# Optimization experiments

Hardware: AMD Instinct MI355X
Metric: run time of the kernel (lower is better)

The kernel has to match this reference:

```python
import jax, jax.numpy as jnp
import jax.scipy.linalg as jsl
import numpy as np

B, T, C = 2, 4096, 1024
HK = HV = 8           # linear_num_key_heads == linear_num_value_heads
DK = DV = 128         # linear_key_head_dim / linear_value_head_dim
CHUNK = 64
CONV_K = 4
KEY_DIM = HK * DK
VAL_DIM = HV * DV
CONV_DIM = 2 * KEY_DIM + VAL_DIM
EPS = 1e-6


def setup_inputs() -> dict:
    key = jax.random.key(0)
    ks = jax.random.split(key, 8)
    s = 0.02
    x = jax.random.normal(ks[0], (B, T, C), jnp.float32)
    W_qkvz = jax.random.normal(ks[1], (C, 2 * KEY_DIM + 2 * VAL_DIM), jnp.float32) * s
    W_ba = jax.random.normal(ks[2], (C, 2 * HV), jnp.float32) * s
    conv_w = jax.random.normal(ks[3], (CONV_DIM, 1, CONV_K), jnp.float32) * 0.3  # depthwise (O,1,K)
    dt_bias = jnp.ones((HV,), jnp.float32)
    A_log = jnp.log(jax.random.uniform(ks[4], (HV,), jnp.float32, 0.5, 8.0))
    norm_weight = jnp.ones((DV,), jnp.float32)
    W_out = jax.random.normal(ks[5], (VAL_DIM, C), jnp.float32) * s
    return {"x": x, "W_qkvz": W_qkvz, "W_ba": W_ba, "conv_w": conv_w,
            "dt_bias": dt_bias, "A_log": A_log, "norm_weight": norm_weight, "W_out": W_out}


def _l2norm(x, eps=EPS):
    return x * jax.lax.rsqrt(jnp.sum(x * x, -1, keepdims=True) + eps)


def _chunk_gated_delta_rule(q, k, v, g, beta, chunk=CHUNK):
    # q,k: (B,T,H,DK); v: (B,T,H,DV); g,beta: (B,T,H)
    q = _l2norm(q)
    k = _l2norm(k)
    tr = lambda x: jnp.swapaxes(x, 1, 2).astype(jnp.float32)  # -> (B,H,T,...)
    q, k, v, g, beta = tr(q), tr(k), tr(v), tr(g), tr(beta)
    b, h, t, dk = k.shape
    dv = v.shape[-1]
    n = t // chunk  # T divisible by chunk (pad_size == 0)
    q = q * (dk ** -0.5)
    v_beta = v * beta[..., None]
    k_beta = k * beta[..., None]
    rs = lambda x: x.reshape(b, h, n, chunk, x.shape[-1])
    q, k, v_beta, k_beta = rs(q), rs(k), rs(v_beta), rs(k_beta)
    g = jnp.cumsum(g.reshape(b, h, n, chunk), axis=-1)
    # decay_mask[..., i, j] = exp(g_i - g_j) for j <= i, else 0
    decay = jnp.tril(jnp.exp(jnp.tril(g[..., :, None] - g[..., None, :])))
    # forward substitution == unit-lower-triangular solve: (I + tri)^{-1}
    tri = jnp.tril(jnp.einsum('bhnck,bhndk->bhncd', k_beta, k) * decay, -1)
    eye = jnp.eye(chunk, dtype=jnp.float32)
    Tm = jsl.solve_triangular(eye + tri, jnp.broadcast_to(eye, tri.shape), lower=True)
    v_new = Tm @ v_beta                                   # (B,H,N,C,DV)
    k_cum = Tm @ (k_beta * jnp.exp(g)[..., None])         # (B,H,N,C,DK)
    keep_low = jnp.tril(jnp.ones((chunk, chunk), bool))

    def step(S, inp):
        q_i, k_i, v_i, kc_i, g_i, dm_i = inp              # (B,H,C,*)
        attn = jnp.where(keep_low, (q_i @ jnp.swapaxes(k_i, -1, -2)) * dm_i, 0.0)
        v_n = v_i - kc_i @ S
        out = (q_i * jnp.exp(g_i)[..., None]) @ S + attn @ v_n
        g_last = g_i[..., -1]
        S = S * jnp.exp(g_last)[..., None, None] + jnp.einsum(
            'bhck,bhcv->bhkv', k_i * jnp.exp(g_last[..., None] - g_i)[..., None], v_n)
        return S, out

    mv = lambda x: jnp.moveaxis(x, 2, 0)                  # chunk axis to front
    S0 = jnp.zeros((b, h, dk, dv), jnp.float32)
    S, outs = jax.lax.scan(step, S0, (mv(q), mv(k), mv(v_new), mv(k_cum), mv(g), mv(decay)))
    out = jnp.moveaxis(outs, 0, 2).reshape(b, h, t, dv)
    return jnp.swapaxes(out, 1, 2), S                     # (B,T,H,DV), (B,H,DK,DV)


def reference(x, W_qkvz, W_ba, conv_w, dt_bias, A_log, norm_weight, W_out):
    Bx, Tx, Cx = x.shape
    ratio = HV // HK
    qkvz = (x @ W_qkvz).reshape(Bx, Tx, HK, 2 * DK + 2 * ratio * DV)
    q, k, v, z = jnp.split(qkvz, [DK, 2 * DK, 2 * DK + ratio * DV], axis=3)
    v = v.reshape(Bx, Tx, HV, DV)
    z = z.reshape(Bx, Tx, HV, DV)
    ba = (x @ W_ba).reshape(Bx, Tx, HK, 2 * ratio)
    b_, a_ = jnp.split(ba, [ratio], axis=3)
    b_ = b_.reshape(Bx, Tx, HV)
    a_ = a_.reshape(Bx, Tx, HV)
    mixed = jnp.concatenate([q.reshape(Bx, Tx, -1), k.reshape(Bx, Tx, -1),
                             v.reshape(Bx, Tx, -1)], axis=-1)
    # causal depthwise conv1d (left pad K-1, take first T)
    xc = jnp.swapaxes(mixed, 1, 2)                        # (B, CONV_DIM, T)
    conv = jax.lax.conv_general_dilated(xc, conv_w, (1,), [(CONV_K - 1, 0)],
                                        dimension_numbers=('NCH', 'OIH', 'NCH'),
                                        feature_group_count=CONV_DIM)
    conv = jnp.swapaxes(jax.nn.silu(conv), 1, 2)          # (B,T,CONV_DIM)
    qc, kc, vc = jnp.split(conv, [KEY_DIM, 2 * KEY_DIM], axis=-1)
    qc = qc.reshape(Bx, Tx, HK, DK)
    kc = kc.reshape(Bx, Tx, HK, DK)
    vc = vc.reshape(Bx, Tx, HV, DV)
    if ratio > 1:
        qc = jnp.repeat(qc, ratio, axis=2)
        kc = jnp.repeat(kc, ratio, axis=2)
    beta = jax.nn.sigmoid(b_)
    g = -jnp.exp(A_log) * jax.nn.softplus(a_ + dt_bias)
    core, _ = _chunk_gated_delta_rule(qc, kc, vc, g, beta)
    # GatedRMSNorm over head_v_dim, gated by silu(z)
    h = core.astype(jnp.float32)
    var = jnp.mean(h * h, -1, keepdims=True)
    h = norm_weight * (h * jax.lax.rsqrt(var + EPS))
    h = h * jax.nn.silu(z.astype(jnp.float32))
    return h.reshape(Bx, Tx, VAL_DIM) @ W_out
```

## Files before the change

kernel.cpp:

```cpp
#include <hip/hip_runtime.h>
#include <cstddef>

#define Bx 2
#define Tn 4096
#define Hh 8

typedef unsigned short u16;
typedef unsigned int u32;
typedef __attribute__((ext_vector_type(8))) short short8;
typedef __attribute__((ext_vector_type(4))) float f32x4;

__device__ __forceinline__ float bf2f(u16 u) {
  u32 x = ((u32)u) << 16;
  return __uint_as_float(x);
}
__device__ __forceinline__ u16 f2bf(float f) {
  u32 x = __float_as_uint(f);
  u32 lsb = (x >> 16) & 1;
  x += 0x7fffu + lsb;
  return (u16)(x >> 16);
}
__device__ __forceinline__ u32 pack2(float a, float b) {
  return (u32)f2bf(a) | ((u32)f2bf(b) << 16);
}
__device__ __forceinline__ short8 cvt8(float4 f0, float4 f1) {
  uint4 p;
  p.x = pack2(f0.x, f0.y);
  p.y = pack2(f0.z, f0.w);
  p.z = pack2(f1.x, f1.y);
  p.w = pack2(f1.z, f1.w);
  return *(short8*)&p;
}
__device__ __forceinline__ void async16(u16* lds, const u16* g) {
  __builtin_amdgcn_global_load_lds((const __attribute__((address_space(1))) void*)g,
                                   (__attribute__((address_space(3))) void*)lds, 16, 0, 0);
}

__global__ __launch_bounds__(256) void conv_bf16(const float* __restrict__ X,
                                                 u16* __restrict__ Xb) {
  int i = (blockIdx.x * 256 + threadIdx.x) * 8;
  float4 v0 = *(const float4*)&X[i];
  float4 v1 = *(const float4*)&X[i + 4];
  uint4 pv;
  pv.x = pack2(v0.x, v0.y);
  pv.y = pack2(v0.z, v0.w);
  pv.z = pack2(v1.x, v1.y);
  pv.w = pack2(v1.z, v1.w);
  *(uint4*)&Xb[i] = pv;
}

__global__ __launch_bounds__(256) void transpose_bf16(const float* __restrict__ W,
                                                      u16* __restrict__ WT,
                                                      int K, int N) {
  __shared__ float tile[64][68];
  int nb = blockIdx.x, kb = blockIdx.y;
  int tid = threadIdx.x;
  int r = tid >> 4, c4 = (tid & 15) * 4;
#pragma unroll
  for (int p = 0; p < 4; p++) {
    int k = kb * 64 + p * 16 + r;
    float4 v = *(const float4*)&W[(size_t)k * N + nb * 64 + c4];
    tile[p * 16 + r][c4] = v.x;
    tile[p * 16 + r][c4 + 1] = v.y;
    tile[p * 16 + r][c4 + 2] = v.z;
    tile[p * 16 + r][c4 + 3] = v.w;
  }
  __syncthreads();
  int rn = tid >> 2, ck = (tid & 3) * 16;
#pragma unroll
  for (int s = 0; s < 2; s++) {
    int k0 = ck + s * 8;
    uint4 pv;
    pv.x = pack2(tile[k0 + 0][rn], tile[k0 + 1][rn]);
    pv.y = pack2(tile[k0 + 2][rn], tile[k0 + 3][rn]);
    pv.z = pack2(tile[k0 + 4][rn], tile[k0 + 5][rn]);
    pv.w = pack2(tile[k0 + 6][rn], tile[k0 + 7][rn]);
    *(uint4*)&WT[(size_t)(nb * 64 + rn) * K + kb * 64 + k0] = pv;
  }
}

template<int EPI>
__global__ __launch_bounds__(256) void gemm_mfma(const u16* __restrict__ A,
                                                 const u16* __restrict__ Bt,
                                                 u16* __restrict__ O1,
                                                 u16* __restrict__ O2,
                                                 float* __restrict__ O3,
                                                 int Nfull) {
  const int K = 1024;
  __shared__ u16 As[128 * 32];
  __shared__ u16 Bs[128 * 32];
  int bn = blockIdx.x, bm = blockIdx.y;
  int tid = threadIdx.x;
  int wave = tid >> 6, lane = tid & 63;
  int wr = wave >> 1, wc = wave & 1;

  f32x4 acc[4][4];
#pragma unroll
  for (int i = 0; i < 4; i++)
#pragma unroll
    for (int j = 0; j < 4; j++) acc[i][j] = (f32x4){0.f, 0.f, 0.f, 0.f};

  const u16* Ab = A + (size_t)(bm * 128 + wave * 32 + (lane >> 2)) * K + (lane & 3) * 8;
  const u16* Bb = Bt + (size_t)(bn * 128 + wave * 32 + (lane >> 2)) * K + (lane & 3) * 8;
  u16* AsW = &As[(wave * 32) * 32];
  u16* BsW = &Bs[(wave * 32) * 32];

  int m_lane = lane & 15, k_lane = (lane >> 4) * 8;
  const u16* arow0 = &As[(wr * 64 + m_lane) * 32 + k_lane];
  const u16* brow0 = &Bs[(wc * 64 + m_lane) * 32 + k_lane];

  for (int kk = 0; kk < K; kk += 32) {
    __syncthreads();
    async16(AsW, Ab + kk);
    async16(AsW + 16 * 32, Ab + 16 * K + kk);
    async16(BsW, Bb + kk);
    async16(BsW + 16 * 32, Bb + 16 * K + kk);
    __syncthreads();
    short8 a[4], b[4];
#pragma unroll
    for (int t = 0; t < 4; t++) a[t] = *(const short8*)(arow0 + t * 16 * 32);
#pragma unroll
    for (int t = 0; t < 4; t++) b[t] = *(const short8*)(brow0 + t * 16 * 32);
#pragma unroll
    for (int i = 0; i < 4; i++)
#pragma unroll
      for (int j = 0; j < 4; j++)
        acc[i][j] = __builtin_amdgcn_mfma_f32_16x16x32_bf16(a[i], b[j], acc[i][j], 0, 0, 0);
  }

  int n0 = bn * 128;
  int cbase = wc * 64 + (lane & 15);
  int rbase = bm * 128 + wr * 64 + ((lane >> 4) * 4);
  if (EPI == 1) {
    int h = n0 >> 9, sub = (n0 >> 7) & 3;
    u16* dst;
    size_t stride;
    if (sub < 3) { dst = O1 + (size_t)(sub * 1024 + h * 128); stride = 3072; }
    else         { dst = O2 + (size_t)(h * 128);              stride = 1024; }
#pragma unroll
    for (int i = 0; i < 4; i++)
#pragma unroll
      for (int j = 0; j < 4; j++)
#pragma unroll
        for (int r = 0; r < 4; r++)
          dst[(size_t)(rbase + i * 16 + r) * stride + cbase + j * 16] = f2bf(acc[i][j][r]);
  } else {
#pragma unroll
    for (int i = 0; i < 4; i++)
#pragma unroll
      for (int j = 0; j < 4; j++)
#pragma unroll
        for (int r = 0; r < 4; r++)
          O3[(size_t)(rbase + i * 16 + r) * Nfull + n0 + cbase + j * 16] = acc[i][j][r];
  }
}

__global__ __launch_bounds__(128) void ba_kernel(const float* __restrict__ x,
                                                 const float* __restrict__ Wba,
                                                 const float* __restrict__ dtb,
                                                 const float* __restrict__ Alog,
                                                 float* __restrict__ betab,
                                                 float* __restrict__ gb) {
  __shared__ float xs[1024];
  __shared__ float part[8][16];
  int row = blockIdx.x, tid = threadIdx.x;
#pragma unroll
  for (int r = 0; r < 2; r++) {
    int f4 = r * 128 + tid;
    *(float4*)&xs[f4 * 4] = *(const float4*)&x[(size_t)row * 1024 + f4 * 4];
  }
  __syncthreads();
  int col = tid & 15, seg = tid >> 4;
  float a = 0.f;
  for (int k = seg * 128; k < seg * 128 + 128; k++) a += xs[k] * Wba[k * 16 + col];
  part[seg][col] = a;
  __syncthreads();
  if (tid < 8) {
    float bval = 0.f, aval = 0.f;
#pragma unroll
    for (int q = 0; q < 8; q++) { bval += part[q][tid * 2]; aval += part[q][tid * 2 + 1]; }
    betab[(size_t)row * 8 + tid] = 1.f / (1.f + expf(-bval));
    float spin = aval + dtb[tid];
    float sp = (spin > 20.f) ? spin : log1pf(expf(spin));
    gb[(size_t)row * 8 + tid] = -expf(Alog[tid]) * sp;
  }
}

__global__ __launch_bounds__(256) void convnorm(const u16* __restrict__ mixed,
                                                const float* __restrict__ cw,
                                                const float* __restrict__ gbuf,
                                                u16* __restrict__ qn,
                                                u16* __restrict__ kn,
                                                u16* __restrict__ kdT) {
  __shared__ __align__(16) u16 sRaw[67 * 128];
  __shared__ __align__(16) u16 sO[64 * 136];
  __shared__ float red_s[256];
  __shared__ float inv_s[64];
  __shared__ float eglc_s[64];
  int n = blockIdx.x, bh = blockIdx.y, type = blockIdx.z;
  int b = bh >> 3, h = bh & 7;
  int t0 = n * 64, tid = threadIdx.x;
  int srow = tid >> 4, scol8 = (tid & 15) * 8;
  int base = type * 1024;

#pragma unroll
  for (int pass = 0; pass < 5; pass++) {
    int r = pass * 16 + srow;
    if (r < 67) {
      int t = t0 - 3 + r;
      uint4 v = make_uint4(0u, 0u, 0u, 0u);
      if (t >= 0) v = *(const uint4*)&mixed[(size_t)(b * Tn + t) * 3072 + base + h * 128 + scol8];
      *(uint4*)&sRaw[r * 128 + scol8] = v;
    }
  }
  if (type == 1 && tid < 64) {
    float gv = gbuf[(size_t)(b * Tn + t0 + tid) * 8 + h];
#pragma unroll
    for (int off = 1; off < 64; off <<= 1) {
      float o = __shfl_up(gv, off, 64);
      if (tid >= off) gv += o;
    }
    float gl = __shfl(gv, 63, 64);
    eglc_s[tid] = expf(gl - gv);
  }
  __syncthreads();

#pragma unroll
  for (int it = 0; it < 32; it++) {
    int idx = it * 256 + tid;
    int i = idx >> 7, d = idx & 127;
    int colw = (base + h * 128 + d) * 4;
    float a = 0.f;
#pragma unroll
    for (int tap = 0; tap < 4; tap++)
      a += bf2f(sRaw[(i + tap) * 128 + d]) * cw[colw + tap];
    a = a / (1.f + expf(-a));
    sO[i * 136 + d] = f2bf(a);
  }
  __syncthreads();
  {
    int i = tid >> 2, p = tid & 3;
    float ss = 0.f;
#pragma unroll
    for (int d = p * 32; d < p * 32 + 32; d += 2) {
      u32 w2 = *(const u32*)&sO[i * 136 + d];
      float a = bf2f(w2 & 0xffff), b2 = bf2f(w2 >> 16);
      ss += a * a + b2 * b2;
    }
    red_s[tid] = ss;
  }
  __syncthreads();
  if (tid < 64) {
    float inv = rsqrtf(red_s[tid * 4] + red_s[tid * 4 + 1] + red_s[tid * 4 + 2] + red_s[tid * 4 + 3] + 1e-6f);
    inv_s[tid] = (type == 0) ? inv * 0.08838834764831845f : inv;
  }
  __syncthreads();
  u16* dstRow = (type == 0 ? qn : kn) + (size_t)(bh * Tn + t0) * 128;
#pragma unroll
  for (int it = 0; it < 16; it++) {
    int idx = it * 256 + tid;
    int i = idx >> 6, d2 = (idx & 63) * 2;
    u32 w2 = *(const u32*)&sO[i * 136 + d2];
    float inv = inv_s[i];
    float q0 = bf2f(w2 & 0xffff) * inv, q1 = bf2f(w2 >> 16) * inv;
    u32 pk = pack2(q0, q1);
    if (type == 1) *(u32*)&sO[i * 136 + d2] = pk;
    *(u32*)&dstRow[(size_t)i * 128 + d2] = pk;
  }
  if (type == 1) {
    __syncthreads();
    const size_t tbase = (size_t)(bh * 64 + n) * 8192;
#pragma unroll
    for (int it = 0; it < 32; it++) {
      int idx = it * 256 + tid;
      int d = idx >> 6, i = idx & 63;
      kdT[tbase + d * 64 + i] = f2bf(bf2f(sO[i * 136 + d]) * eglc_s[i]);
    }
  }
}

__global__ __launch_bounds__(256) void prep(const u16* __restrict__ mixed,
                                            const float* __restrict__ cw,
                                            const float* __restrict__ gbuf,
                                            const float* __restrict__ betabuf,
                                            u16* qbuf,
                                            u16* kbuf,
                                            u16* __restrict__ vnT,
                                            u16* __restrict__ attn,
                                            float* __restrict__ egl) {
  __shared__ __align__(16) u16 sKn[64 * 136];
  __shared__ __align__(16) u16 sQn[64 * 136];
  __shared__ __align__(16) u16 sRawV[67 * 128];
  __shared__ float gc_s[64], egc_s[64], bet_s[64];
  float* triL = (float*)sQn;

  int n = blockIdx.x, bh = blockIdx.y;
  int b = bh >> 3, h = bh & 7;
  int t0 = n * 64;
  int tid = threadIdx.x;
  const int rowg0 = b * Tn + t0;
  const int rowh0 = bh * Tn + t0;
  const size_t tbase = (size_t)(bh * 64 + n) * 8192;

  int wv = tid >> 6, lane = tid & 63;
  int m16 = lane & 15, q8 = (lane >> 4) * 8, qr = (lane >> 4) * 4;
  int srow = tid >> 4, scol8 = (tid & 15) * 8;

#pragma unroll
  for (int it = 0; it < 4; it++) {
    int idx = it * 256 + tid;
    int i = idx >> 4, c8 = (idx & 15) * 8;
    *(uint4*)&sQn[i * 136 + c8] = *(const uint4*)&qbuf[(size_t)(rowh0 + i) * 128 + c8];
    *(uint4*)&sKn[i * 136 + c8] = *(const uint4*)&kbuf[(size_t)(rowh0 + i) * 128 + c8];
  }
#pragma unroll
  for (int pass = 0; pass < 5; pass++) {
    int r = pass * 16 + srow;
    if (r < 67) {
      int t = t0 - 3 + r;
      uint4 v = make_uint4(0u, 0u, 0u, 0u);
      if (t >= 0) v = *(const uint4*)&mixed[(size_t)(b * Tn + t) * 3072 + 2048 + h * 128 + scol8];
      *(uint4*)&sRawV[r * 128 + scol8] = v;
    }
  }
  if (tid < 64) {
    float gv = gbuf[(size_t)(rowg0 + tid) * 8 + h];
    float bv = betabuf[(size_t)(rowg0 + tid) * 8 + h];
#pragma unroll
    for (int off = 1; off < 64; off <<= 1) {
      float o = __shfl_up(gv, off, 64);
      if (tid >= off) gv += o;
    }
    float gl = __shfl(gv, 63, 64);
    gc_s[tid] = gv;
    egc_s[tid] = expf(gv);
    bet_s[tid] = bv;
    if (tid == 63) egl[bh * 64 + n] = expf(gl);
  }
  __syncthreads();

#pragma unroll
  for (int it = 0; it < 16; it++) {
    int idx = it * 256 + tid;
    int i = idx >> 6, d2 = (idx & 63) * 2;
    u32 w2 = *(const u32*)&sQn[i * 136 + d2];
    float e = egc_s[i];
    *(u32*)&qbuf[(size_t)(rowh0 + i) * 128 + d2] =
        pack2(bf2f(w2 & 0xffff) * e, bf2f(w2 >> 16) * e);
  }
  {
    short8 qa[4];
#pragma unroll
    for (int kt = 0; kt < 4; kt++)
      qa[kt] = *(const short8*)&sQn[(wv * 16 + m16) * 136 + kt * 32 + q8];
    u16* atp = attn + (size_t)(bh * 64 + n) * 4096;
#pragma unroll
    for (int jt = 0; jt < 4; jt++) {
      int j = jt * 16 + m16;
      if (jt <= wv) {
        f32x4 o = (f32x4){0.f, 0.f, 0.f, 0.f};
#pragma unroll
        for (int kt = 0; kt < 4; kt++) {
          short8 kb = *(const short8*)&sKn[(jt * 16 + m16) * 136 + kt * 32 + q8];
          o = __builtin_amdgcn_mfma_f32_16x16x32_bf16(qa[kt], kb, o, 0, 0, 0);
        }
#pragma unroll
        for (int r = 0; r < 4; r++) {
          int i = wv * 16 + qr + r;
          float val = (j <= i) ? o[r] * expf(gc_s[i] - gc_s[j]) : 0.f;
          atp[i * 64 + j] = f2bf(val);
        }
      } else {
#pragma unroll
        for (int r = 0; r < 4; r++) atp[(wv * 16 + qr + r) * 64 + j] = 0;
      }
    }
  }
  __syncthreads();
  {
    short8 ka[4];
#pragma unroll
    for (int kt = 0; kt < 4; kt++)
      ka[kt] = *(const short8*)&sKn[(wv * 16 + m16) * 136 + kt * 32 + q8];
#pragma unroll
    for (int jt = 0; jt < 4; jt++) {
      int j = jt * 16 + m16;
      if (jt <= wv) {
        f32x4 o = (f32x4){0.f, 0.f, 0.f, 0.f};
#pragma unroll
        for (int kt = 0; kt < 4; kt++) {
          short8 kb = *(const short8*)&sKn[(jt * 16 + m16) * 136 + kt * 32 + q8];
          o = __builtin_amdgcn_mfma_f32_16x16x32_bf16(ka[kt], kb, o, 0, 0, 0);
        }
#pragma unroll
        for (int r = 0; r < 4; r++) {
          int i = wv * 16 + qr + r;
          triL[i * 64 + j] = (j < i) ? bet_s[i] * expf(gc_s[i] - gc_s[j]) * o[r] : 0.f;
        }
      } else if (jt == wv + 1) {
#pragma unroll
        for (int r = 0; r < 4; r++) triL[(wv * 16 + qr + r) * 64 + j] = 0.f;
      }
    }
  }
  __syncthreads();

  {
    int mat = tid >> 7, c = tid & 127;
    float x[64];
    if (mat == 0) {
#pragma unroll
      for (int i = 0; i < 64; i++)
        x[i] = bf2f(sKn[i * 136 + c]) * bet_s[i] * egc_s[i];
    } else {
      float cwv[4];
      int colw = (2048 + h * 128 + c) * 4;
#pragma unroll
      for (int tap = 0; tap < 4; tap++) cwv[tap] = cw[colw + tap];
#pragma unroll
      for (int i = 0; i < 64; i++) {
        float a = 0.f;
#pragma unroll
        for (int tap = 0; tap < 4; tap++)
          a += bf2f(sRawV[(i + tap) * 128 + c]) * cwv[tap];
        a = a / (1.f + expf(-a));
        x[i] = a * bet_s[i];
      }
    }
#pragma unroll
    for (int i = 1; i < 64; i++) {
      float s0 = 0.f, s1 = 0.f, s2 = 0.f, s3 = 0.f;
#pragma unroll
      for (int l4 = 0; l4 < (i + 3) / 4; l4++) {
        float4 t4 = *(float4*)&triL[i * 64 + l4 * 4];
        s0 += t4.x * x[l4 * 4 + 0];
        s1 += t4.y * x[l4 * 4 + 1];
        s2 += t4.z * x[l4 * 4 + 2];
        s3 += t4.w * x[l4 * 4 + 3];
      }
      x[i] = x[i] - ((s0 + s1) + (s2 + s3));
    }
    if (mat == 0) {
#pragma unroll
      for (int i = 0; i < 64; i++) kbuf[(size_t)(rowh0 + i) * 128 + c] = f2bf(-x[i]);
    } else {
#pragma unroll
      for (int i = 0; i < 64; i += 2)
        *(u32*)&vnT[tbase + c * 64 + i] = pack2(x[i], x[i + 1]);
    }
  }
}

__device__ __forceinline__ void stage_half(int w, u16* ldsb,
                                           const u16* __restrict__ qgc,
                                           const u16* __restrict__ kcc,
                                           const u16* __restrict__ ktc,
                                           const u16* __restrict__ atc,
                                           const u16* __restrict__ vtc,
                                           int lane) {
  int l8 = lane * 8;
  if (w == 0) {
#pragma unroll
    for (int i = 0; i < 16; i++) {
      int p = i * 512 + l8;
      async16(ldsb + i * 512, qgc + (p ^ ((((p >> 7) & 15)) << 3)));
    }
#pragma unroll
    for (int i = 0; i < 8; i++) {
      int p = i * 512 + l8;
      async16(ldsb + 24576 + i * 512, atc + (p ^ ((((p >> 6) & 7)) << 3)));
    }
#pragma unroll
    for (int i = 0; i < 2; i++) {
      int p = i * 512 + l8;
      async16(ldsb + 28672 + i * 512, vtc + (p ^ ((((p >> 6) & 7)) << 3)));
    }
  } else {
#pragma unroll
    for (int i = 0; i < 16; i++) {
      int p = i * 512 + l8;
      async16(ldsb + 8192 + i * 512, kcc + (p ^ ((((p >> 7) & 15)) << 3)));
    }
#pragma unroll
    for (int i = 0; i < 16; i++) {
      int p = i * 512 + l8;
      async16(ldsb + 16384 + i * 512, ktc + (p ^ ((((p >> 6) & 7)) << 3)));
    }
  }
}

__global__ __launch_bounds__(128, 1) void scan_mfma(const u16* __restrict__ qg,
                                                    const u16* __restrict__ kdT,
                                                    const u16* __restrict__ vnT,
                                                    const u16* __restrict__ kcum,
                                                    const u16* __restrict__ attn,
                                                    const float* __restrict__ egl,
                                                    float* __restrict__ core) {
  extern __shared__ __align__(16) u16 dyn[];
  __shared__ float ST[16 * 132];
  __shared__ float VN[16 * 68];
  int blk = blockIdx.x;
  int bh = blk & 15, tile = blk >> 4;
  int dv0 = tile * 16;
  int b = bh >> 3, h = bh & 7;
  int tid = threadIdx.x;
  int w = tid >> 6, lane = tid & 63;
  int q = lane >> 4, col = lane & 15;
  int c7 = col & 7;
  int tw0 = w * 4;

  for (int r = tid; r < 16 * 132; r += 128) ST[r] = 0.f;
  float egAll = egl[bh * 64 + lane];

  const u16* qg_base = qg + (size_t)bh * Tn * 128;
  const u16* kc_base = kcum + (size_t)bh * Tn * 128;
  const u16* kt_base = kdT + (size_t)bh * 64 * 8192;
  const u16* at_base = attn + (size_t)bh * 64 * 4096;
  const u16* vt_base = vnT + (size_t)bh * 64 * 8192 + dv0 * 64;

  stage_half(w, dyn, qg_base, kc_base, kt_base, at_base, vt_base, lane);
  asm volatile("s_waitcnt vmcnt(0)" ::: "memory");
  __syncthreads();

  for (int n = 0; n < 64; n++) {
    u16* buf = dyn + (n & 1) * 29696;

    short8 kcf[8], qgf[8], ktf[8], atf[4];
    uint2 vtf[2];
#pragma unroll
    for (int m = 0; m < 2; m++) {
      int mt = w * 2 + m;
#pragma unroll
      for (int kt = 0; kt < 4; kt++) {
        kcf[m * 4 + kt] = *(const short8*)&buf[8192 + (mt * 16 + col) * 128 +
                                               (((kt * 4 + q) ^ col) << 3)];
        qgf[m * 4 + kt] = *(const short8*)&buf[(mt * 16 + col) * 128 +
                                               (((kt * 4 + q) ^ col) << 3)];
      }
#pragma unroll
      for (int kt2 = 0; kt2 < 2; kt2++)
        atf[m * 2 + kt2] = *(const short8*)&buf[24576 + (mt * 16 + col) * 64 +
                                                (((kt2 * 4 + q) ^ c7) << 3)];
      vtf[m] = *(const uint2*)&buf[28672 + col * 64 +
                                   (((mt * 2 + (q >> 1)) ^ c7) << 3) + (q & 1) * 4];
    }
#pragma unroll
    for (int t = 0; t < 4; t++)
#pragma unroll
      for (int kt2 = 0; kt2 < 2; kt2++)
        ktf[t * 2 + kt2] = *(const short8*)&buf[16384 + ((tw0 + t) * 16 + col) * 64 +
                                                (((kt2 * 4 + q) ^ c7) << 3)];
    short8 sb[4];
#pragma unroll
    for (int kt = 0; kt < 4; kt++) {
      float4 f0 = *(float4*)&ST[col * 132 + kt * 32 + q * 8];
      float4 f1 = *(float4*)&ST[col * 132 + kt * 32 + q * 8 + 4];
      sb[kt] = cvt8(f0, f1);
    }
    float4 stu[4];
#pragma unroll
    for (int t = 0; t < 4; t++) stu[t] = *(float4*)&ST[col * 132 + (tw0 + t) * 16 + q * 4];

    if (n < 63) {
      stage_half(w, dyn + ((n + 1) & 1) * 29696,
                 qg_base + (size_t)(n + 1) * 8192,
                 kc_base + (size_t)(n + 1) * 8192,
                 kt_base + (size_t)(n + 1) * 8192,
                 at_base + (size_t)(n + 1) * 4096,
                 vt_base + (size_t)(n + 1) * 8192, lane);
    }
    float eg = __shfl(egAll, n, 64);

#pragma unroll
    for (int m = 0; m < 2; m++) {
      f32x4 a0;
      a0[0] = bf2f(vtf[m].x & 0xffff); a0[1] = bf2f(vtf[m].x >> 16);
      a0[2] = bf2f(vtf[m].y & 0xffff); a0[3] = bf2f(vtf[m].y >> 16);
#pragma unroll
      for (int kt = 0; kt < 4; kt++)
        a0 = __builtin_amdgcn_mfma_f32_16x16x32_bf16(kcf[m * 4 + kt], sb[kt], a0, 0, 0, 0);
      *(f32x4*)&VN[col * 68 + (w * 2 + m) * 16 + q * 4] = a0;
    }
    asm volatile("s_waitcnt lgkmcnt(0)" ::: "memory");
    __builtin_amdgcn_s_barrier();
    __builtin_amdgcn_sched_barrier(0);

    short8 vb[2];
#pragma unroll
    for (int kt2 = 0; kt2 < 2; kt2++) {
      float4 f0 = *(float4*)&VN[col * 68 + kt2 * 32 + q * 8];
      float4 f1 = *(float4*)&VN[col * 68 + kt2 * 32 + q * 8 + 4];
      vb[kt2] = cvt8(f0, f1);
    }

#pragma unroll
    for (int t = 0; t < 4; t++) {
      f32x4 s0;
      s0[0] = stu[t].x * eg; s0[1] = stu[t].y * eg;
      s0[2] = stu[t].z * eg; s0[3] = stu[t].w * eg;
#pragma unroll
      for (int kt2 = 0; kt2 < 2; kt2++)
        s0 = __builtin_amdgcn_mfma_f32_16x16x32_bf16(ktf[t * 2 + kt2], vb[kt2], s0, 0, 0, 0);
      *(f32x4*)&ST[col * 132 + (tw0 + t) * 16 + q * 4] = s0;
    }

#pragma unroll
    for (int m = 0; m < 2; m++) {
      f32x4 o = (f32x4){0.f, 0.f, 0.f, 0.f};
#pragma unroll
      for (int kt = 0; kt < 4; kt++)
        o = __builtin_amdgcn_mfma_f32_16x16x32_bf16(qgf[m * 4 + kt], sb[kt], o, 0, 0, 0);
#pragma unroll
      for (int kt2 = 0; kt2 < 2; kt2++)
        o = __builtin_amdgcn_mfma_f32_16x16x32_bf16(atf[m * 2 + kt2], vb[kt2], o, 0, 0, 0);
      size_t rowb = (size_t)(b * Tn) + n * 64 + (w * 2 + m) * 16 + q * 4;
#pragma unroll
      for (int r2 = 0; r2 < 4; r2++)
        core[(rowb + r2) * 1024 + h * 128 + dv0 + col] = o[r2];
    }

    asm volatile("s_waitcnt vmcnt(8) lgkmcnt(0)" ::: "memory");
    __builtin_amdgcn_s_barrier();
    __builtin_amdgcn_sched_barrier(0);
  }
}

__global__ __launch_bounds__(256) void gnorm(const float* __restrict__ core,
                                             const u16* __restrict__ z,
                                             const float* __restrict__ nw,
                                             u16* __restrict__ coreb) {
  __shared__ float red[256];
  __shared__ float rstd[8];
  int row = blockIdx.x, tid = threadIdx.x;
  float4 c4 = *(const float4*)&core[(size_t)row * 1024 + tid * 4];
  uint2 zl = *(const uint2*)&z[(size_t)row * 1024 + tid * 4];
  float4 z4;
  z4.x = bf2f(zl.x & 0xffff); z4.y = bf2f(zl.x >> 16);
  z4.z = bf2f(zl.y & 0xffff); z4.w = bf2f(zl.y >> 16);
  red[tid] = c4.x * c4.x + c4.y * c4.y + c4.z * c4.z + c4.w * c4.w;
  __syncthreads();
  if (tid < 8) {
    float s = 0.f;
    for (int t2 = tid * 32; t2 < tid * 32 + 32; t2++) s += red[t2];
    rstd[tid] = rsqrtf(s * (1.f / 128.f) + 1e-6f);
  }
  __syncthreads();
  float rs = rstd[tid >> 5];
  int d0 = (tid * 4) & 127;
  float4 w4 = *(const float4*)&nw[d0];
  float4 o;
  o.x = c4.x * rs * w4.x * (z4.x / (1.f + expf(-z4.x)));
  o.y = c4.y * rs * w4.y * (z4.y / (1.f + expf(-z4.y)));
  o.z = c4.z * rs * w4.z * (z4.z / (1.f + expf(-z4.z)));
  o.w = c4.w * rs * w4.w * (z4.w / (1.f + expf(-z4.w)));
  uint2 pv;
  pv.x = pack2(o.x, o.y);
  pv.y = pack2(o.z, o.w);
  *(uint2*)&coreb[(size_t)row * 1024 + tid * 4] = pv;
}

extern "C" void kernel_launch(void* const* d_in, const int* in_sizes, int n_in,
                              void* d_out, int out_size, void* d_ws, size_t ws_size,
                              hipStream_t stream) {
  const float* x     = (const float*)d_in[0];
  const float* Wqkvz = (const float*)d_in[1];
  const float* Wba   = (const float*)d_in[2];
  const float* convw = (const float*)d_in[3];
  const float* dtb   = (const float*)d_in[4];
  const float* Alog  = (const float*)d_in[5];
  const float* nw    = (const float*)d_in[6];
  const float* Wout  = (const float*)d_in[7];
  float* out = (float*)d_out;

  char* w = (char*)d_ws;
  u16*   mixed = (u16*)w;
  float* core  = (float*)w;
  u16*   coreb = (u16*)(w + 33554432);
  u16*   zb    = (u16*)(w + 50331648);
  float* betab = (float*)(w + 67108864);
  float* gb    = (float*)(w + 67371008);
  u16*   qgB   = (u16*)(w + 67633152);
  u16*   xb    = (u16*)(w + 67633152);
  u16*   kdTB  = (u16*)(w + 84410368);
  u16*   WqT   = (u16*)(w + 84410368);
  u16*   vnTB  = (u16*)(w + 101187584);
  u16*   kcB   = (u16*)(w + 117964800);
  u16*   WoT   = (u16*)(w + 117964800);
  u16*   atB   = (u16*)(w + 134742016);
  float* eglB  = (float*)(w + 143130624);

  static bool attr_set = false;
  if (!attr_set) {
    hipFuncSetAttribute(reinterpret_cast<const void*>(scan_mfma),
                        hipFuncAttributeMaxDynamicSharedMemorySize, 118784);
    attr_set = true;
  }

  conv_bf16<<<dim3(4096), 256, 0, stream>>>(x, xb);
  transpose_bf16<<<dim3(64, 16), 256, 0, stream>>>(Wqkvz, WqT, 1024, 4096);
  gemm_mfma<1><<<dim3(32, 64), 256, 0, stream>>>(xb, WqT, mixed, zb, nullptr, 4096);
  ba_kernel<<<dim3(8192), 128, 0, stream>>>(x, Wba, dtb, Alog, betab, gb);
  convnorm<<<dim3(64, 16, 2), 256, 0, stream>>>(mixed, convw, gb, qgB, kcB, kdTB);
  prep<<<dim3(64, 16), 256, 0, stream>>>(mixed, convw, gb, betab, qgB, kcB, vnTB, atB, eglB);
  scan_mfma<<<dim3(128), 128, 118784, stream>>>(qgB, kdTB, vnTB, kcB, atB, eglB, core);
  transpose_bf16<<<dim3(16, 16), 256, 0, stream>>>(Wout, WoT, 1024, 1024);
  gnorm<<<dim3(8192), 256, 0, stream>>>(core, zb, nw, coreb);
  gemm_mfma<0><<<dim3(8, 64), 256, 0, stream>>>(coreb, WoT, nullptr, nullptr, out, 1024);
}
```

Measured before the change: 446.3 us.

## Split scan work across four waves and keep state in registers with bf16 LDS

The sequential chunk-scan kernel now runs 4 waves per block instead of 2, so each wave owns one 16-row tile and half as many state tiles, and staging of the next chunk is split four ways. The fp32 recurrent state is kept in registers across iterations, and only a bf16, swizzled copy goes to LDS for the other waves to read. This removes the per-iteration fp32 LDS reads and conversions and shortens each wave's serial dependency chain. The cost is more barrier participants and extra bf16 packing work.

```diff
diff --git a/kernel.cpp b/kernel.cpp
--- a/kernel.cpp
+++ b/kernel.cpp
@@ -451,20 +451,33 @@
   }
 }
 
-__device__ __forceinline__ void stage_half(int w, u16* ldsb,
-                                           const u16* __restrict__ qgc,
-                                           const u16* __restrict__ kcc,
-                                           const u16* __restrict__ ktc,
-                                           const u16* __restrict__ atc,
-                                           const u16* __restrict__ vtc,
-                                           int lane) {
+__device__ __forceinline__ void stage_quarter(int w, u16* ldsb,
+                                              const u16* __restrict__ qgc,
+                                              const u16* __restrict__ kcc,
+                                              const u16* __restrict__ ktc,
+                                              const u16* __restrict__ atc,
+                                              const u16* __restrict__ vtc,
+                                              int lane) {
   int l8 = lane * 8;
   if (w == 0) {
+#pragma unroll
+    for (int i = 0; i < 16; i++) {
+      int p = i * 512 + l8;
+      async16(ldsb + 8192 + i * 512, kcc + (p ^ ((((p >> 7) & 15)) << 3)));
+    }
+  } else if (w == 1) {
+#pragma unroll
+    for (int i = 0; i < 16; i++) {
+      int p = i * 512 + l8;
+      async16(ldsb + 16384 + i * 512, ktc + (p ^ ((((p >> 6) & 7)) << 3)));
+    }
+  } else if (w == 2) {
 #pragma unroll
     for (int i = 0; i < 16; i++) {
       int p = i * 512 + l8;
       async16(ldsb + i * 512, qgc + (p ^ ((((p >> 7) & 15)) << 3)));
     }
+  } else {
 #pragma unroll
     for (int i = 0; i < 8; i++) {
       int p = i * 512 + l8;
@@ -475,21 +488,10 @@
       int p = i * 512 + l8;
       async16(ldsb + 28672 + i * 512, vtc + (p ^ ((((p >> 6) & 7)) << 3)));
     }
-  } else {
-#pragma unroll
-    for (int i = 0; i < 16; i++) {
-      int p = i * 512 + l8;
-      async16(ldsb + 8192 + i * 512, kcc + (p ^ ((((p >> 7) & 15)) << 3)));
-    }
-#pragma unroll
-    for (int i = 0; i < 16; i++) {
-      int p = i * 512 + l8;
-      async16(ldsb + 16384 + i * 512, ktc + (p ^ ((((p >> 6) & 7)) << 3)));
-    }
-  }
-}
-
-__global__ __launch_bounds__(128, 1) void scan_mfma(const u16* __restrict__ qg,
+  }
+}
+
+__global__ __launch_bounds__(256, 1) void scan_mfma(const u16* __restrict__ qg,
                                                     const u16* __restrict__ kdT,
                                                     const u16* __restrict__ vnT,
                                                     const u16* __restrict__ kcum,
@@ -497,8 +499,8 @@
                                                     const float* __restrict__ egl,
                                                     float* __restrict__ core) {
   extern __shared__ __align__(16) u16 dyn[];
-  __shared__ float ST[16 * 132];
-  __shared__ float VN[16 * 68];
+  __shared__ __align__(16) u16 STb[16 * 128];
+  __shared__ __align__(16) u16 VNb[16 * 64];
   int blk = blockIdx.x;
   int bh = blk & 15, tile = blk >> 4;
   int dv0 = tile * 16;
@@ -507,10 +509,13 @@
   int w = tid >> 6, lane = tid & 63;
   int q = lane >> 4, col = lane & 15;
   int c7 = col & 7;
-  int tw0 = w * 4;
-
-  for (int r = tid; r < 16 * 132; r += 128) ST[r] = 0.f;
+  int qh = q >> 1, ql = q & 1;
+
+  for (int r = tid; r < 16 * 128 / 2; r += 256) ((u32*)STb)[r] = 0u;
   float egAll = egl[bh * 64 + lane];
+
+  f32x4 st0 = (f32x4){0.f, 0.f, 0.f, 0.f};
+  f32x4 st1 = (f32x4){0.f, 0.f, 0.f, 0.f};
 
   const u16* qg_base = qg + (size_t)bh * Tn * 128;
   const u16* kc_base = kcum + (size_t)bh * Tn * 128;
@@ -518,68 +523,52 @@
   const u16* at_base = attn + (size_t)bh * 64 * 4096;
   const u16* vt_base = vnT + (size_t)bh * 64 * 8192 + dv0 * 64;
 
-  stage_half(w, dyn, qg_base, kc_base, kt_base, at_base, vt_base, lane);
+  stage_quarter(w, dyn, qg_base, kc_base, kt_base, at_base, vt_base, lane);
   asm volatile("s_waitcnt vmcnt(0)" ::: "memory");
   __syncthreads();
 
   for (int n = 0; n < 64; n++) {
     u16* buf = dyn + (n & 1) * 29696;
 
-    short8 kcf[8], qgf[8], ktf[8], atf[4];
-    uint2 vtf[2];
-#pragma unroll
-    for (int m = 0; m < 2; m++) {
-      int mt = w * 2 + m;
-#pragma unroll
-      for (int kt = 0; kt < 4; kt++) {
-        kcf[m * 4 + kt] = *(const short8*)&buf[8192 + (mt * 16 + col) * 128 +
-                                               (((kt * 4 + q) ^ col) << 3)];
-        qgf[m * 4 + kt] = *(const short8*)&buf[(mt * 16 + col) * 128 +
-                                               (((kt * 4 + q) ^ col) << 3)];
-      }
-#pragma unroll
-      for (int kt2 = 0; kt2 < 2; kt2++)
-        atf[m * 2 + kt2] = *(const short8*)&buf[24576 + (mt * 16 + col) * 64 +
+    short8 kcf[4], qgf[4], ktf[4], atf[2], sb[4];
+    uint2 vtf;
+#pragma unroll
+    for (int kt = 0; kt < 4; kt++) {
+      kcf[kt] = *(const short8*)&buf[8192 + (w * 16 + col) * 128 + (((kt * 4 + q) ^ col) << 3)];
+      qgf[kt] = *(const short8*)&buf[(w * 16 + col) * 128 + (((kt * 4 + q) ^ col) << 3)];
+      sb[kt] = *(const short8*)&STb[col * 128 + (((kt * 4 + q) ^ col) << 3)];
+    }
+#pragma unroll
+    for (int kt2 = 0; kt2 < 2; kt2++) {
+      atf[kt2] = *(const short8*)&buf[24576 + (w * 16 + col) * 64 + (((kt2 * 4 + q) ^ c7) << 3)];
+#pragma unroll
+      for (int t = 0; t < 2; t++)
+        ktf[t * 2 + kt2] = *(const short8*)&buf[16384 + ((w * 2 + t) * 16 + col) * 64 +
                                                 (((kt2 * 4 + q) ^ c7) << 3)];
-      vtf[m] = *(const uint2*)&buf[28672 + col * 64 +
-                                   (((mt * 2 + (q >> 1)) ^ c7) << 3) + (q & 1) * 4];
-    }
-#pragma unroll
-    for (int t = 0; t < 4; t++)
-#pragma unroll
-      for (int kt2 = 0; kt2 < 2; kt2++)
-        ktf[t * 2 + kt2] = *(const short8*)&buf[16384 + ((tw0 + t) * 16 + col) * 64 +
-                                                (((kt2 * 4 + q) ^ c7) << 3)];
-    short8 sb[4];
-#pragma unroll
-    for (int kt = 0; kt < 4; kt++) {
-      float4 f0 = *(float4*)&ST[col * 132 + kt * 32 + q * 8];
-      float4 f1 = *(float4*)&ST[col * 132 + kt * 32 + q * 8 + 4];
-      sb[kt] = cvt8(f0, f1);
-    }
-    float4 stu[4];
-#pragma unroll
-    for (int t = 0; t < 4; t++) stu[t] = *(float4*)&ST[col * 132 + (tw0 + t) * 16 + q * 4];
+    }
+    vtf = *(const uint2*)&buf[28672 + col * 64 + (((w * 2 + qh) ^ c7) << 3) + ql * 4];
 
     if (n < 63) {
-      stage_half(w, dyn + ((n + 1) & 1) * 29696,
-                 qg_base + (size_t)(n + 1) * 8192,
-                 kc_base + (size_t)(n + 1) * 8192,
-                 kt_base + (size_t)(n + 1) * 8192,
-                 at_base + (size_t)(n + 1) * 4096,
-                 vt_base + (size_t)(n + 1) * 8192, lane);
+      stage_quarter(w, dyn + ((n + 1) & 1) * 29696,
+                    qg_base + (size_t)(n + 1) * 8192,
+                    kc_base + (size_t)(n + 1) * 8192,
+                    kt_base + (size_t)(n + 1) * 8192,
+                    at_base + (size_t)(n + 1) * 4096,
+                    vt_base + (size_t)(n + 1) * 8192, lane);
     }
     float eg = __shfl(egAll, n, 64);
 
-#pragma unroll
-    for (int m = 0; m < 2; m++) {
+    {
       f32x4 a0;
-      a0[0] = bf2f(vtf[m].x & 0xffff); a0[1] = bf2f(vtf[m].x >> 16);
-      a0[2] = bf2f(vtf[m].y & 0xffff); a0[3] = bf2f(vtf[m].y >> 16);
+      a0[0] = bf2f(vtf.x & 0xffff); a0[1] = bf2f(vtf.x >> 16);
+      a0[2] = bf2f(vtf.y & 0xffff); a0[3] = bf2f(vtf.y >> 16);
 #pragma unroll
       for (int kt = 0; kt < 4; kt++)
-        a0 = __builtin_amdgcn_mfma_f32_16x16x32_bf16(kcf[m * 4 + kt], sb[kt], a0, 0, 0, 0);
-      *(f32x4*)&VN[col * 68 + (w * 2 + m) * 16 + q * 4] = a0;
+        a0 = __builtin_amdgcn_mfma_f32_16x16x32_bf16(kcf[kt], sb[kt], a0, 0, 0, 0);
+      uint2 pk;
+      pk.x = pack2(a0[0], a0[1]);
+      pk.y = pack2(a0[2], a0[3]);
+      *(uint2*)&VNb[col * 64 + (((w * 2 + qh) ^ c7) << 3) + ql * 4] = pk;
     }
     asm volatile("s_waitcnt lgkmcnt(0)" ::: "memory");
     __builtin_amdgcn_s_barrier();
@@ -587,39 +576,47 @@
 
     short8 vb[2];
 #pragma unroll
-    for (int kt2 = 0; kt2 < 2; kt2++) {
-      float4 f0 = *(float4*)&VN[col * 68 + kt2 * 32 + q * 8];
-      float4 f1 = *(float4*)&VN[col * 68 + kt2 * 32 + q * 8 + 4];
-      vb[kt2] = cvt8(f0, f1);
-    }
-
-#pragma unroll
-    for (int t = 0; t < 4; t++) {
+    for (int kt2 = 0; kt2 < 2; kt2++)
+      vb[kt2] = *(const short8*)&VNb[col * 64 + (((kt2 * 4 + q) ^ c7) << 3)];
+
+    {
       f32x4 s0;
-      s0[0] = stu[t].x * eg; s0[1] = stu[t].y * eg;
-      s0[2] = stu[t].z * eg; s0[3] = stu[t].w * eg;
+      s0[0] = st0[0] * eg; s0[1] = st0[1] * eg; s0[2] = st0[2] * eg; s0[3] = st0[3] * eg;
+      s0 = __builtin_amdgcn_mfma_f32_16x16x32_bf16(ktf[0], vb[0], s0, 0, 0, 0);
+      s0 = __builtin_amdgcn_mfma_f32_16x16x32_bf16(ktf[1], vb[1], s0, 0, 0, 0);
+      st0 = s0;
+      uint2 pk;
+      pk.x = pack2(s0[0], s0[1]);
+      pk.y = pack2(s0[2], s0[3]);
+      *(uint2*)&STb[col * 128 + ((((w * 2 + 0) * 2 + qh) ^ col) << 3) + ql * 4] = pk;
+    }
+    {
+      f32x4 s1;
+      s1[0] = st1[0] * eg; s1[1] = st1[1] * eg; s1[2] = st1[2] * eg; s1[3] = st1[3] * eg;
+      s1 = __builtin_amdgcn_mfma_f32_16x16x32_bf16(ktf[2], vb[0], s1, 0, 0, 0);
+      s1 = __builtin_amdgcn_mfma_f32_16x16x32_bf16(ktf[3], vb[1], s1, 0, 0, 0);
+      st1 = s1;
+      uint2 pk;
+      pk.x = pack2(s1[0], s1[1]);
+      pk.y = pack2(s1[2], s1[3]);
+      *(uint2*)&STb[col * 128 + ((((w * 2 + 1) * 2 + qh) ^ col) << 3) + ql * 4] = pk;
+    }
+
+    {
+      f32x4 o = (f32x4){0.f, 0.f, 0.f, 0.f};
+#pragma unroll
+      for (int kt = 0; kt < 4; kt++)
+        o = __builtin_amdgcn_mfma_f32_16x16x32_bf16(qgf[kt], sb[kt], o, 0, 0, 0);
 #pragma unroll
       for (int kt2 = 0; kt2 < 2; kt2++)
-        s0 = __builtin_amdgcn_mfma_f32_16x16x32_bf16(ktf[t * 2 + kt2], vb[kt2], s0, 0, 0, 0);
-      *(f32x4*)&ST[col * 132 + (tw0 + t) * 16 + q * 4] = s0;
-    }
-
-#pragma unroll
-    for (int m = 0; m < 2; m++) {
-      f32x4 o = (f32x4){0.f, 0.f, 0.f, 0.f};
-#pragma unroll
-      for (int kt = 0; kt < 4; kt++)
-        o = __builtin_amdgcn_mfma_f32_16x16x32_bf16(qgf[m * 4 + kt], sb[kt], o, 0, 0, 0);
-#pragma unroll
-      for (int kt2 = 0; kt2 < 2; kt2++)
-        o = __builtin_amdgcn_mfma_f32_16x16x32_bf16(atf[m * 2 + kt2], vb[kt2], o, 0, 0, 0);
-      size_t rowb = (size_t)(b * Tn) + n * 64 + (w * 2 + m) * 16 + q * 4;
+        o = __builtin_amdgcn_mfma_f32_16x16x32_bf16(atf[kt2], vb[kt2], o, 0, 0, 0);
+      size_t rowb = (size_t)(b * Tn) + n * 64 + w * 16 + q * 4;
 #pragma unroll
       for (int r2 = 0; r2 < 4; r2++)
         core[(rowb + r2) * 1024 + h * 128 + dv0 + col] = o[r2];
     }
 
-    asm volatile("s_waitcnt vmcnt(8) lgkmcnt(0)" ::: "memory");
+    asm volatile("s_waitcnt vmcnt(4) lgkmcnt(0)" ::: "memory");
     __builtin_amdgcn_s_barrier();
     __builtin_amdgcn_sched_barrier(0);
   }
@@ -702,7 +699,7 @@
   ba_kernel<<<dim3(8192), 128, 0, stream>>>(x, Wba, dtb, Alog, betab, gb);
   convnorm<<<dim3(64, 16, 2), 256, 0, stream>>>(mixed, convw, gb, qgB, kcB, kdTB);
   prep<<<dim3(64, 16), 256, 0, stream>>>(mixed, convw, gb, betab, qgB, kcB, vnTB, atB, eglB);
-  scan_mfma<<<dim3(128), 128, 118784, stream>>>(qgB, kdTB, vnTB, kcB, atB, eglB, core);
+  scan_mfma<<<dim3(128), 256, 118784, stream>>>(qgB, kdTB, vnTB, kcB, atB, eglB, core);
   transpose_bf16<<<dim3(16, 16), 256, 0, stream>>>(Wout, WoT, 1024, 1024);
   gnorm<<<dim3(8192), 256, 0, stream>>>(core, zb, nw, coreb);
   gemm_mfma<0><<<dim3(8, 64), 256, 0, stream>>>(coreb, WoT, nullptr, nullptr, out, 1024);
```

Measured after the change: 418.6 us. 6.2% less time.
